# Kernel optimization log

Measured on AMD Instinct MI355X. Metric: run time of the kernel, lower is better.

## Reference

```python
import jax, jax.numpy as jnp
import numpy as np

N_RF = 25   # contour integration RF extent (must be odd, 7-55)
N_CH = 96   # AlexNet conv1 feature maps


def _get_coaligned_masks(weights_type, rf_len, non_overlapping_rfs=True):
    """Faithful numpy replication of the manually-defined coalignment masks."""
    half_rf = rf_len // 2
    kernel = np.zeros((N_CH, rf_len, rf_len), dtype=np.float32)
    step = 3 if non_overlapping_rfs else 1
    pre = list(range(0, half_rf, step))
    post = list(range(half_rf + step, rf_len, step))
    kernel[10, pre, half_rf] = 1
    kernel[10, post, half_rf] = 1
    if weights_type != 'enhance':
        kernel[10, half_rf, pre] = -1
        kernel[10, half_rf, post] = -1
    kernel[5, half_rf, pre] = 1
    kernel[5, half_rf, post] = 1
    if weights_type != 'enhance':
        kernel[5, pre, half_rf] = -1
        kernel[5, post, half_rf] = -1
    kernel[54, (1, 4, 6, 9, 15, 17, 20, 23), (8, 9, 10, 11, 13, 14, 15, 16)] = 1
    kernel[64, list(range(0, half_rf, 3)), list(range(0, half_rf, 3))] = 1
    kernel[64, list(range(half_rf + 3, rf_len, 3)), list(range(half_rf + 3, rf_len, 3))] = 1
    if weights_type != 'enhance':
        kernel[64, list(range(rf_len - 1, half_rf, -3)), list(range(0, half_rf, 3))] = -1
        kernel[64, list(range(half_rf - 3, -1, -3)), list(range(half_rf + 3, rf_len, 3))] = -1
    kernel[67, :, :] = np.copy(kernel[54, :, :])
    kernel[78, (1, 3, 7, 10, 14, 17, 21, 23), (17, 16, 14, 13, 11, 10, 8, 7)] = 1
    return kernel


def setup_inputs() -> dict:
    key = jax.random.key(0)
    x = jax.random.normal(key, (128, 55, 55, N_CH), dtype=jnp.float32)  # NHWC, AlexNet conv1 output
    kernel = jnp.asarray(_get_coaligned_masks('enhance_and_suppress', N_RF))  # [ch, n, n]
    return {"x": x, "kernel": kernel}


def reference(x, kernel):
    # The per-(i,j) python loop in the original is exactly a per-channel (depthwise)
    # cross-correlation with the fixed mask kernel, SAME padding (n//2 each side),
    # followed by (identity) activation and residual add.
    ch = x.shape[-1]
    k = jnp.transpose(kernel, (1, 2, 0))[:, :, None, :]  # [n, n, 1, ch] HWIO depthwise
    lateral = jax.lax.conv_general_dilated(
        x, k,
        window_strides=(1, 1),
        padding='SAME',
        dimension_numbers=('NHWC', 'HWIO', 'NHWC'),
        feature_group_count=ch,
    )
    # activation is linear (None) -> identity
    return lateral + x
```

## Files before the change

### kernel.cpp

```cpp
#include <hip/hip_runtime.h>

#define NCH   96
#define RF    25
#define HALF  12
#define HW    55
#define PLANE (HW * HW)
#define CAP   32
#define MAXA  6
#define SROWS 38
#define LDSW  56
#define SPLANE (SROWS * HW)
#define LATP  (14 * HW)

#define WS_META_OFF (NCH * 4 + NCH * CAP * 4 * 2)

__global__ __launch_bounds__(1024) void prep_all(
        const float* __restrict__ kern, int* __restrict__ counts,
        int* __restrict__ tap_off, float* __restrict__ tap_w,
        int* __restrict__ meta) {
    __shared__ int scnt[NCH];
    const int wave = threadIdx.x >> 6;
    const int lane = threadIdx.x & 63;
    for (int c = wave; c < NCH; c += 16) {
        const float* kc = kern + c * (RF * RF);
        int base = 0;
        for (int seg = 0; seg < RF * RF; seg += 64) {
            const int i = seg + lane;
            const float w = (i < RF * RF) ? kc[i] : 0.0f;
            const unsigned long long m = __ballot(w != 0.0f);
            const int pos = base + __popcll(m & ((1ull << lane) - 1ull));
            if (w != 0.0f && pos < CAP) {
                const int dy = i / RF, dx = i - dy * RF;
                tap_off[c * CAP + pos] = (dy << 8) | dx;
                tap_w[c * CAP + pos]   = w;
            }
            base += __popcll(m);
        }
        if (lane == 0) { counts[c] = base; scnt[c] = base; }
    }
    __syncthreads();
    if (threadIdx.x == 0) {
        int na = 0;
        bool fallback = false;
        for (int ch = 0; ch < NCH; ++ch) {
            if (scnt[ch] > 0) {
                if (scnt[ch] > CAP) fallback = true;
                if (na < MAXA) meta[1 + na] = ch;
                ++na;
            }
        }
        if (na > MAXA) fallback = true;
        meta[0] = fallback ? 999 : na;
        for (int a = (na > MAXA ? 0 : na); a < MAXA; ++a) meta[1 + a] = 0;
    }
}

__global__ __launch_bounds__(1024, 8) void contour_tile(
        const float* __restrict__ x, const float* __restrict__ kern,
        const int* __restrict__ counts, const int* __restrict__ tap_off,
        const float* __restrict__ tap_w, const int* __restrict__ meta,
        float* __restrict__ out) {
    __shared__ float sh[MAXA][SROWS][LDSW];
    __shared__ float latf[MAXA * LATP];
    __shared__ float tw[MAXA][CAP];
    __shared__ int   toff[MAXA][CAP];
    __shared__ int   tcnt[MAXA];
    __shared__ int   chA[MAXA];
    __shared__ signed char c2a[NCH];

    const int tid  = threadIdx.x;
    const int b    = blockIdx.x;
    const int xcd  = b & 7;
    const int s    = b >> 3;
    const int n    = xcd + ((s >> 2) << 3);
    const int q    = s & 3;
    const int y0   = q * 14;
    const int rows = (q < 3) ? 14 : 13;
    const int npx  = rows * HW;

    const float* xn = x   + (size_t)n * (PLANE * NCH);
    float*       on = out + (size_t)n * (PLANE * NCH);

    const int na = meta[0];
    const bool fast = (na <= MAXA);

    if (tid < NCH) c2a[tid] = -1;
    __syncthreads();
    if (fast) {
        if (tid < MAXA) {
            const int c = (tid < na) ? meta[1 + tid] : -1;
            chA[tid]  = c;
            tcnt[tid] = (c >= 0) ? counts[c] : 0;
        }
        if (tid < na) c2a[meta[1 + tid]] = (signed char)tid;
        if (tid >= 64 && tid < 64 + MAXA * CAP) {
            const int a = (tid - 64) / CAP, t = (tid - 64) % CAP;
            const int c = (a < na) ? meta[1 + a] : 0;
            toff[a][t] = tap_off[c * CAP + t];
            tw[a][t]   = tap_w[c * CAP + t];
        }
    }
    __syncthreads();

    if (fast) {
        const int totA = na * SPLANE;
        for (int idx = tid; idx < totA; idx += 1024) {
            const int a   = idx / SPLANE;
            const int rem = idx - a * SPLANE;
            const int sr  = rem / HW;
            const int col = rem - sr * HW;
            const int gy  = y0 - HALF + sr;
            float v = 0.0f;
            if ((unsigned)gy < (unsigned)HW)
                v = xn[(size_t)(gy * HW + col) * NCH + chA[a]];
            sh[a][sr][col] = v;
        }
        __syncthreads();

        const int totC = na * LATP;
        for (int idx = tid; idx < totC; idx += 1024) {
            const int a   = idx / LATP;
            const int p   = idx - a * LATP;
            const int r   = p / HW;
            const int col = p - r * HW;
            const int cnt = tcnt[a];
            float acc = 0.0f;
            for (int t = 0; t < cnt; ++t) {
                const int off = toff[a][t];
                const float w = tw[a][t];
                const int dy = off >> 8, dx = off & 255;
                const int xx = col + dx - HALF;
                const bool ok = (unsigned)xx < (unsigned)HW;
                const int  xc = min(max(xx, 0), HW - 1);
                const float vv = sh[a][r + dy][xc];
                acc += ok ? w * vv : 0.0f;
            }
            latf[idx] = acc;
        }
        __syncthreads();

        if (tid < 1008) {
            const int g     = tid % 24;
            const int pslot = tid / 24;
            const int a0 = c2a[g * 4 + 0];
            const int a1 = c2a[g * 4 + 1];
            const int a2 = c2a[g * 4 + 2];
            const int a3 = c2a[g * 4 + 3];
            const bool anyact = (a0 >= 0) | (a1 >= 0) | (a2 >= 0) | (a3 >= 0);
            const float4* xs = (const float4*)(xn + (size_t)y0 * HW * NCH);
            float4*       os = (float4*)      (on + (size_t)y0 * HW * NCH);
            #pragma unroll 2
            for (int p = pslot; p < npx; p += 42) {
                const int idx = p * 24 + g;
                float4 v = xs[idx];
                if (anyact) {
                    if (a0 >= 0) v.x += latf[a0 * LATP + p];
                    if (a1 >= 0) v.y += latf[a1 * LATP + p];
                    if (a2 >= 0) v.z += latf[a2 * LATP + p];
                    if (a3 >= 0) v.w += latf[a3 * LATP + p];
                }
                os[idx] = v;
            }
        }
    } else {
        for (int idx = tid; idx < npx * (NCH / 4); idx += 1024) {
            const int g   = idx % (NCH / 4);
            const int pix = idx / (NCH / 4);
            const int r   = pix / HW;
            const int col = pix - r * HW;
            const int py  = y0 + r;
            const size_t pbase = (size_t)(py * HW + col) * NCH;
            const float4 xv = *(const float4*)(xn + pbase + g * 4);
            float acc[4] = {xv.x, xv.y, xv.z, xv.w};
            for (int kk = 0; kk < 4; ++kk) {
                const int c = g * 4 + kk;
                const int cnt = counts[c];
                if (cnt == 0) continue;
                float aa = 0.0f;
                if (cnt <= CAP) {
                    for (int t = 0; t < cnt; ++t) {
                        const int off = tap_off[c * CAP + t];
                        const float w = tap_w[c * CAP + t];
                        const int dy = off >> 8, dx = off & 255;
                        const int yy = py + dy - HALF;
                        const int xx = col + dx - HALF;
                        if ((unsigned)yy < (unsigned)HW && (unsigned)xx < (unsigned)HW)
                            aa += w * xn[(size_t)(yy * HW + xx) * NCH + c];
                    }
                } else {
                    for (int dy = 0; dy < RF; ++dy)
                        for (int dx = 0; dx < RF; ++dx) {
                            const float w = kern[(c * RF + dy) * RF + dx];
                            if (w == 0.0f) continue;
                            const int yy = py + dy - HALF;
                            const int xx = col + dx - HALF;
                            if ((unsigned)yy < (unsigned)HW && (unsigned)xx < (unsigned)HW)
                                aa += w * xn[(size_t)(yy * HW + xx) * NCH + c];
                        }
                }
                acc[kk] += aa;
            }
            *(float4*)(on + pbase + g * 4) = make_float4(acc[0], acc[1], acc[2], acc[3]);
        }
    }
}

extern "C" void kernel_launch(void* const* d_in, const int* in_sizes, int n_in,
                              void* d_out, int out_size, void* d_ws, size_t ws_size,
                              hipStream_t stream) {
    const float* x    = (const float*)d_in[0];
    const float* kern = (const float*)d_in[1];
    float* out = (float*)d_out;

    int*   counts  = (int*)d_ws;
    int*   tap_off = (int*)((char*)d_ws + NCH * 4);
    float* tap_w   = (float*)((char*)d_ws + NCH * 4 + NCH * CAP * 4);
    int*   meta    = (int*)((char*)d_ws + WS_META_OFF);

    prep_all<<<1, 1024, 0, stream>>>(kern, counts, tap_off, tap_w, meta);

    contour_tile<<<512, 1024, 0, stream>>>(x, kern, counts, tap_off, tap_w, meta, out);
}
```

Measured before the change: 343.8 us.

## Split work per image by channel half and stream copy during gather

Result: slower. 400.6 us (+16.5%).

```diff
diff --git a/kernel.cpp b/kernel.cpp
--- a/kernel.cpp
+++ b/kernel.cpp
@@ -6,11 +6,8 @@
 #define HW    55
 #define PLANE (HW * HW)
 #define CAP   32
-#define MAXA  6
-#define SROWS 38
-#define LDSW  56
-#define SPLANE (SROWS * HW)
-#define LATP  (14 * HW)
+#define MAXA  4
+#define NGRP  12
 
 #define WS_META_OFF (NCH * 4 + NCH * CAP * 4 * 2)
 
@@ -40,140 +37,153 @@
     }
     __syncthreads();
     if (threadIdx.x == 0) {
-        int na = 0;
+        int na[2] = {0, 0};
         bool fallback = false;
         for (int ch = 0; ch < NCH; ++ch) {
             if (scnt[ch] > 0) {
                 if (scnt[ch] > CAP) fallback = true;
-                if (na < MAXA) meta[1 + na] = ch;
-                ++na;
-            }
-        }
-        if (na > MAXA) fallback = true;
-        meta[0] = fallback ? 999 : na;
-        for (int a = (na > MAXA ? 0 : na); a < MAXA; ++a) meta[1 + a] = 0;
+                const int h = ch / 48;
+                if (na[h] < MAXA) meta[3 + h * MAXA + na[h]] = ch;
+                ++na[h];
+            }
+        }
+        if (na[0] > MAXA || na[1] > MAXA) fallback = true;
+        meta[0] = fallback ? 999 : 0;
+        meta[1] = na[0] < MAXA ? na[0] : MAXA;
+        meta[2] = na[1] < MAXA ? na[1] : MAXA;
+        for (int h = 0; h < 2; ++h)
+            for (int i = na[h]; i < MAXA; ++i) meta[3 + h * MAXA + i] = 0;
     }
 }
 
-__global__ __launch_bounds__(1024, 8) void contour_tile(
+__global__ __launch_bounds__(1024, 4) void contour_img(
         const float* __restrict__ x, const float* __restrict__ kern,
         const int* __restrict__ counts, const int* __restrict__ tap_off,
         const float* __restrict__ tap_w, const int* __restrict__ meta,
         float* __restrict__ out) {
-    __shared__ float sh[MAXA][SROWS][LDSW];
-    __shared__ float latf[MAXA * LATP];
+    __shared__ float sh[MAXA][HW][56];
+    __shared__ float lat[MAXA * PLANE];
     __shared__ float tw[MAXA][CAP];
     __shared__ int   toff[MAXA][CAP];
     __shared__ int   tcnt[MAXA];
-    __shared__ int   chA[MAXA];
-    __shared__ signed char c2a[NCH];
-
-    const int tid  = threadIdx.x;
-    const int b    = blockIdx.x;
-    const int xcd  = b & 7;
-    const int s    = b >> 3;
-    const int n    = xcd + ((s >> 2) << 3);
-    const int q    = s & 3;
-    const int y0   = q * 14;
-    const int rows = (q < 3) ? 14 : 13;
-    const int npx  = rows * HW;
+    __shared__ signed char c2l[48];
+    __shared__ int   wrNow[NGRP];
+    __shared__ int   dsec[3];
+    __shared__ int   ndsS;
+
+    const int tid = threadIdx.x;
+    const int b   = blockIdx.x;
+    const int n   = b >> 1;
+    const int h   = b & 1;
 
     const float* xn = x   + (size_t)n * (PLANE * NCH);
     float*       on = out + (size_t)n * (PLANE * NCH);
 
-    const int na = meta[0];
-    const bool fast = (na <= MAXA);
-
-    if (tid < NCH) c2a[tid] = -1;
+    const bool fast = (meta[0] != 999);
+    const int  na   = fast ? meta[1 + h] : 0;
+
+    if (tid < 48) c2l[tid] = -1;
     __syncthreads();
     if (fast) {
-        if (tid < MAXA) {
-            const int c = (tid < na) ? meta[1 + tid] : -1;
-            chA[tid]  = c;
-            tcnt[tid] = (c >= 0) ? counts[c] : 0;
-        }
-        if (tid < na) c2a[meta[1 + tid]] = (signed char)tid;
+        if (tid < na) {
+            const int c = meta[3 + h * MAXA + tid];
+            tcnt[tid] = counts[c];
+            c2l[c - h * 48] = (signed char)tid;
+        }
         if (tid >= 64 && tid < 64 + MAXA * CAP) {
             const int a = (tid - 64) / CAP, t = (tid - 64) % CAP;
-            const int c = (a < na) ? meta[1 + a] : 0;
+            const int c = (a < na) ? meta[3 + h * MAXA + a] : h * 48;
             toff[a][t] = tap_off[c * CAP + t];
             tw[a][t]   = tap_w[c * CAP + t];
         }
     }
     __syncthreads();
+    if (fast && tid == 0) {
+        int nds = 0;
+        for (int s = 0; s < 3; ++s) {
+            bool act = false;
+            for (int c = s * 16; c < s * 16 + 16; ++c) act |= (c2l[c] >= 0);
+            for (int g = s * 4; g < s * 4 + 4; ++g) wrNow[g] = act ? 0 : 1;
+            if (act) dsec[nds++] = s;
+        }
+        ndsS = nds;
+    }
+    __syncthreads();
 
     if (fast) {
-        const int totA = na * SPLANE;
-        for (int idx = tid; idx < totA; idx += 1024) {
-            const int a   = idx / SPLANE;
-            const int rem = idx - a * SPLANE;
-            const int sr  = rem / HW;
-            const int col = rem - sr * HW;
-            const int gy  = y0 - HALF + sr;
-            float v = 0.0f;
-            if ((unsigned)gy < (unsigned)HW)
-                v = xn[(size_t)(gy * HW + col) * NCH + chA[a]];
-            sh[a][sr][col] = v;
+        const float4* xs = (const float4*)xn;
+        float4*       os = (float4*)on;
+        const int base = h * NGRP;
+
+        #pragma unroll 2
+        for (int idx = tid; idx < PLANE * NGRP; idx += 1024) {
+            const int px = idx / NGRP;
+            const int gg = idx - px * NGRP;
+            const int fi = px * 24 + base + gg;
+            const float4 v = xs[fi];
+            const int r = px / HW, col = px - r * HW;
+            const int lc = gg * 4;
+            const int a0 = c2l[lc + 0], a1 = c2l[lc + 1];
+            const int a2 = c2l[lc + 2], a3 = c2l[lc + 3];
+            if (a0 >= 0) sh[a0][r][col] = v.x;
+            if (a1 >= 0) sh[a1][r][col] = v.y;
+            if (a2 >= 0) sh[a2][r][col] = v.z;
+            if (a3 >= 0) sh[a3][r][col] = v.w;
+            if (wrNow[gg]) os[fi] = v;
         }
         __syncthreads();
 
-        const int totC = na * LATP;
-        for (int idx = tid; idx < totC; idx += 1024) {
-            const int a   = idx / LATP;
-            const int p   = idx - a * LATP;
-            const int r   = p / HW;
-            const int col = p - r * HW;
+        for (int idx = tid; idx < na * PLANE; idx += 1024) {
+            const int a = idx / PLANE, p = idx - a * PLANE;
+            const int r = p / HW, col = p - r * HW;
             const int cnt = tcnt[a];
             float acc = 0.0f;
             for (int t = 0; t < cnt; ++t) {
                 const int off = toff[a][t];
                 const float w = tw[a][t];
-                const int dy = off >> 8, dx = off & 255;
-                const int xx = col + dx - HALF;
-                const bool ok = (unsigned)xx < (unsigned)HW;
-                const int  xc = min(max(xx, 0), HW - 1);
-                const float vv = sh[a][r + dy][xc];
+                const int yy = r   + (off >> 8)  - HALF;
+                const int xx = col + (off & 255) - HALF;
+                const bool ok = ((unsigned)yy < (unsigned)HW) &
+                                ((unsigned)xx < (unsigned)HW);
+                const int yc = min(max(yy, 0), HW - 1);
+                const int xc = min(max(xx, 0), HW - 1);
+                const float vv = sh[a][yc][xc];
                 acc += ok ? w * vv : 0.0f;
             }
-            latf[idx] = acc;
+            lat[idx] = acc;
         }
         __syncthreads();
 
-        if (tid < 1008) {
-            const int g     = tid % 24;
-            const int pslot = tid / 24;
-            const int a0 = c2a[g * 4 + 0];
-            const int a1 = c2a[g * 4 + 1];
-            const int a2 = c2a[g * 4 + 2];
-            const int a3 = c2a[g * 4 + 3];
-            const bool anyact = (a0 >= 0) | (a1 >= 0) | (a2 >= 0) | (a3 >= 0);
-            const float4* xs = (const float4*)(xn + (size_t)y0 * HW * NCH);
-            float4*       os = (float4*)      (on + (size_t)y0 * HW * NCH);
-            #pragma unroll 2
-            for (int p = pslot; p < npx; p += 42) {
-                const int idx = p * 24 + g;
-                float4 v = xs[idx];
-                if (anyact) {
-                    if (a0 >= 0) v.x += latf[a0 * LATP + p];
-                    if (a1 >= 0) v.y += latf[a1 * LATP + p];
-                    if (a2 >= 0) v.z += latf[a2 * LATP + p];
-                    if (a3 >= 0) v.w += latf[a3 * LATP + p];
-                }
-                os[idx] = v;
-            }
+        const int nds  = ndsS;
+        const int tot2 = PLANE * nds * 4;
+        for (int idx = tid; idx < tot2; idx += 1024) {
+            const int px  = idx / (nds * 4);
+            const int rem = idx - px * (nds * 4);
+            const int d = rem >> 2, j = rem & 3;
+            const int gg = dsec[d] * 4 + j;
+            const int fi = px * 24 + base + gg;
+            float4 v = xs[fi];
+            const int lc = gg * 4;
+            const int a0 = c2l[lc + 0], a1 = c2l[lc + 1];
+            const int a2 = c2l[lc + 2], a3 = c2l[lc + 3];
+            if (a0 >= 0) v.x += lat[a0 * PLANE + px];
+            if (a1 >= 0) v.y += lat[a1 * PLANE + px];
+            if (a2 >= 0) v.z += lat[a2 * PLANE + px];
+            if (a3 >= 0) v.w += lat[a3 * PLANE + px];
+            os[fi] = v;
         }
     } else {
-        for (int idx = tid; idx < npx * (NCH / 4); idx += 1024) {
-            const int g   = idx % (NCH / 4);
-            const int pix = idx / (NCH / 4);
-            const int r   = pix / HW;
-            const int col = pix - r * HW;
-            const int py  = y0 + r;
-            const size_t pbase = (size_t)(py * HW + col) * NCH;
-            const float4 xv = *(const float4*)(xn + pbase + g * 4);
+        const float4* xs = (const float4*)xn;
+        float4*       os = (float4*)on;
+        for (int idx = tid; idx < PLANE * NGRP; idx += 1024) {
+            const int px = idx / NGRP;
+            const int gg = idx - px * NGRP;
+            const int r  = px / HW, col = px - r * HW;
+            const int fi = px * 24 + h * NGRP + gg;
+            const float4 xv = xs[fi];
             float acc[4] = {xv.x, xv.y, xv.z, xv.w};
             for (int kk = 0; kk < 4; ++kk) {
-                const int c = g * 4 + kk;
+                const int c = h * 48 + gg * 4 + kk;
                 const int cnt = counts[c];
                 if (cnt == 0) continue;
                 float aa = 0.0f;
@@ -182,9 +192,10 @@
                         const int off = tap_off[c * CAP + t];
                         const float w = tap_w[c * CAP + t];
                         const int dy = off >> 8, dx = off & 255;
-                        const int yy = py + dy - HALF;
+                        const int yy = r   + dy - HALF;
                         const int xx = col + dx - HALF;
-                        if ((unsigned)yy < (unsigned)HW && (unsigned)xx < (unsigned)HW)
+                        if ((unsigned)yy < (unsigned)HW &&
+                            (unsigned)xx < (unsigned)HW)
                             aa += w * xn[(size_t)(yy * HW + xx) * NCH + c];
                     }
                 } else {
@@ -192,15 +203,16 @@
                         for (int dx = 0; dx < RF; ++dx) {
                             const float w = kern[(c * RF + dy) * RF + dx];
                             if (w == 0.0f) continue;
-                            const int yy = py + dy - HALF;
+                            const int yy = r   + dy - HALF;
                             const int xx = col + dx - HALF;
-                            if ((unsigned)yy < (unsigned)HW && (unsigned)xx < (unsigned)HW)
+                            if ((unsigned)yy < (unsigned)HW &&
+                                (unsigned)xx < (unsigned)HW)
                                 aa += w * xn[(size_t)(yy * HW + xx) * NCH + c];
                         }
                 }
                 acc[kk] += aa;
             }
-            *(float4*)(on + pbase + g * 4) = make_float4(acc[0], acc[1], acc[2], acc[3]);
+            os[fi] = make_float4(acc[0], acc[1], acc[2], acc[3]);
         }
     }
 }
@@ -219,5 +231,5 @@
 
     prep_all<<<1, 1024, 0, stream>>>(kern, counts, tap_off, tap_w, meta);
 
-    contour_tile<<<512, 1024, 0, stream>>>(x, kern, counts, tap_off, tap_w, meta, out);
+    contour_img<<<256, 1024, 0, stream>>>(x, kern, counts, tap_off, tap_w, meta, out);
 }
```
